# Performance work log

Hardware: AMD Instinct MI355X
Metric: run time of the kernel (lower is better)

The kernel has to match this reference:

```python
import jax, jax.numpy as jnp
import numpy as np

N = 10000        # nodes
E = 160000       # edges (avg degree 16)
WIDTH = 32       # node hidden width
KER_W = 256      # kernel MLP hidden width
KER_IN = 6       # edge feature dim
DEPTH = 4        # message-passing iterations


def setup_inputs() -> dict:
    key = jax.random.key(0)
    ks = jax.random.split(key, 12)
    def w(k, shape, fan_in):
        return jax.random.normal(k, shape, jnp.float32) * (1.0 / np.sqrt(fan_in)).astype(np.float32)
    return {
        "x": jax.random.normal(ks[0], (N, 1), jnp.float32),
        "edge_index": jax.random.randint(ks[1], (2, E), 0, N),
        "edge_attr": jax.random.uniform(ks[2], (E, KER_IN), dtype=jnp.float32),
        # fc1: Linear(1, WIDTH)
        "fc1_w": w(ks[3], (1, WIDTH), 1), "fc1_b": jnp.zeros((WIDTH,), jnp.float32),
        # kernel DenseNet: KER_IN -> KER_W -> KER_W -> WIDTH^2 (ReLU between, none after last)
        "k1_w": w(ks[4], (KER_IN, KER_W), KER_IN), "k1_b": jnp.zeros((KER_W,), jnp.float32),
        "k2_w": w(ks[5], (KER_W, KER_W), KER_W), "k2_b": jnp.zeros((KER_W,), jnp.float32),
        "k3_w": w(ks[6], (KER_W, WIDTH * WIDTH), KER_W), "k3_b": jnp.zeros((WIDTH * WIDTH,), jnp.float32),
        # NNConv root weight + bias
        "root_w": w(ks[7], (WIDTH, WIDTH), WIDTH), "conv_b": jnp.zeros((WIDTH,), jnp.float32),
        # fc2: Linear(WIDTH, 1)
        "fc2_w": w(ks[8], (WIDTH, 1), WIDTH), "fc2_b": jnp.zeros((1,), jnp.float32),
    }


def reference(x, edge_index, edge_attr, fc1_w, fc1_b, k1_w, k1_b, k2_w, k2_b,
              k3_w, k3_b, root_w, conv_b, fc2_w, fc2_b):
    src, dst = edge_index[0], edge_index[1]  # messages flow src -> dst

    # Per-edge kernel weights (edge_attr is constant across depth -> compute once).
    h = jax.nn.relu(edge_attr @ k1_w + k1_b)
    h = jax.nn.relu(h @ k2_w + k2_b)
    W_e = (h @ k3_w + k3_b).reshape(E, WIDTH, WIDTH)  # [E, in, out]

    # Degree for scatter-mean (avoid div by zero).
    deg = jax.ops.segment_sum(jnp.ones((E,), jnp.float32), dst, num_segments=N)
    inv_deg = (1.0 / jnp.maximum(deg, 1.0))[:, None]

    h_node = x @ fc1_w + fc1_b  # [N, WIDTH]
    for _ in range(DEPTH):
        msg = jnp.einsum('ei,eio->eo', h_node[src], W_e)              # gather + per-edge GEMM
        agg = jax.ops.segment_sum(msg, dst, num_segments=N) * inv_deg  # scatter-mean
        h_node = jax.nn.relu(agg + h_node @ root_w + conv_b)
    return h_node @ fc2_w + fc2_b  # [N, 1]
```

## Files before the change

kernel.cpp:

```cpp
#include <hip/hip_runtime.h>
#include <hip/hip_fp16.h>

#define NNODE 10000
#define NEDGE 160000
#define W32 32
#define BSTR 40
#define PANEL_F16 10240
#define PANEL3_F16 5120
#define UB_TILES 20000
#define HB_STR 268
#define TB_STR 1036

typedef _Float16 f16;
typedef _Float16 f16x4 __attribute__((ext_vector_type(4)));
typedef _Float16 f16x8 __attribute__((ext_vector_type(8)));
typedef float f32x4 __attribute__((ext_vector_type(4)));

__device__ __forceinline__ void stage_panel(f16* lds, const f16* g, int w, int lane) {
    #pragma unroll
    for (int i = 0; i < 5; ++i) {
        int slot = w * 320 + i * 64 + lane;
        __builtin_amdgcn_global_load_lds(
            (const __attribute__((address_space(1))) unsigned int*)(g + (size_t)slot * 8),
            (__attribute__((address_space(3))) unsigned int*)(lds + (size_t)(w * 320 + i * 64) * 8),
            16, 0, 0);
    }
}

__device__ __forceinline__ void stage_panel10k(f16* lds, const f16* g, int w, int lane) {
    #pragma unroll
    for (int i = 0; i < 2; ++i) {
        int base = i * 256 + w * 64;
        __builtin_amdgcn_global_load_lds(
            (const __attribute__((address_space(1))) unsigned int*)(g + (size_t)(base + lane) * 8),
            (__attribute__((address_space(3))) unsigned int*)(lds + (size_t)base * 8),
            16, 0, 0);
    }
    if (w < 2) {
        int base = 512 + w * 64;
        __builtin_amdgcn_global_load_lds(
            (const __attribute__((address_space(1))) unsigned int*)(g + (size_t)(base + lane) * 8),
            (__attribute__((address_space(3))) unsigned int*)(lds + (size_t)base * 8),
            16, 0, 0);
    }
}

__global__ __launch_bounds__(256) void pack_k1(const float* __restrict__ k1w, f16* __restrict__ k1p) {
    int t = blockIdx.x * 256 + threadIdx.x;
    int j = t / BSTR, c = t % BSTR;
    k1p[t] = (c < 6) ? (f16)k1w[c * 256 + j] : (f16)0.f;
}
__global__ __launch_bounds__(256) void pack_k2(const float* __restrict__ k2w, f16* __restrict__ k2p) {
    int t = blockIdx.x * 256 + threadIdx.x;
    int kk = t / PANEL_F16, r = t % PANEL_F16;
    int j = r / BSTR, c = r % BSTR;
    k2p[t] = (c < 32) ? (f16)k2w[(size_t)(kk * 32 + c) * 256 + j] : (f16)0.f;
}
__global__ __launch_bounds__(256) void pack_k3(const float* __restrict__ k3w, f16* __restrict__ k3p) {
    int t = blockIdx.x * 256 + threadIdx.x;
    int p = t / PANEL3_F16, r = t % PANEL3_F16;
    int np = p >> 3, kk = p & 7;
    int j = r / BSTR, c = r % BSTR;
    k3p[t] = (c < 32) ? (f16)k3w[(size_t)(kk * 32 + c) * 1024 + np * 128 + j] : (f16)0.f;
}
__global__ __launch_bounds__(256) void pack_k3t(const float* __restrict__ k3w, f16* __restrict__ k3t) {
    int t = blockIdx.x * 256 + threadIdx.x;
    int q = t / BSTR, i = t % BSTR;
    int o = q >> 8, c = q & 255;
    k3t[t] = (i < 32) ? (f16)k3w[(size_t)c * 1024 + i * 32 + o] : (f16)0.f;
}

__global__ __launch_bounds__(256) void h2_kernel(
    const float* __restrict__ ea,
    const f16* __restrict__ k1p, const float* __restrict__ k1b,
    const f16* __restrict__ k2p, const float* __restrict__ k2b,
    f16* __restrict__ h2c, int e_start, const int* __restrict__ remap)
{
    __shared__ __align__(16) f16 bls[2][256 * BSTR];
    __shared__ __align__(16) f16 ea_s[64 * BSTR];
    __shared__ __align__(16) f16 hbuf[64 * HB_STR];

    const int t = threadIdx.x, w = t >> 6, lane = t & 63, quad = lane >> 4, l15 = lane & 15;
    const int el0 = blockIdx.x * 64;
    const int e0 = e_start + el0;

    stage_panel(bls[0], k1p, w, lane);
    for (int i = t; i < 64 * BSTR; i += 256) {
        int e = i / BSTR, c = i % BSTR;
        ea_s[i] = (f16)((c < 6) ? ea[(size_t)(e0 + e) * 6 + c] : 0.f);
    }
    __syncthreads();

    f16x8 a1 = *(const f16x8*)&ea_s[(w * 16 + l15) * BSTR + quad * 8];
    f32x4 acc[16];
    #pragma unroll
    for (int nt = 0; nt < 16; ++nt) { float b = k1b[nt * 16 + l15]; acc[nt] = (f32x4){b, b, b, b}; }
    stage_panel(bls[1], k2p, w, lane);
    #pragma unroll
    for (int nt = 0; nt < 16; ++nt) {
        f16x8 bf = *(const f16x8*)&bls[0][(nt * 16 + l15) * BSTR + quad * 8];
        acc[nt] = __builtin_amdgcn_mfma_f32_16x16x32_f16(a1, bf, acc[nt], 0, 0, 0);
    }
    #pragma unroll
    for (int nt = 0; nt < 16; ++nt)
        #pragma unroll
        for (int r = 0; r < 4; ++r)
            hbuf[(w * 16 + quad * 4 + r) * HB_STR + nt * 16 + l15] = (f16)fmaxf(acc[nt][r], 0.f);
    __syncthreads();

    f16x8 a2[8];
    #pragma unroll
    for (int kk = 0; kk < 8; ++kk)
        a2[kk] = *(const f16x8*)&hbuf[(w * 16 + l15) * HB_STR + kk * 32 + quad * 8];
    #pragma unroll
    for (int nt = 0; nt < 16; ++nt) { float b = k2b[nt * 16 + l15]; acc[nt] = (f32x4){b, b, b, b}; }
    for (int kk = 0; kk < 8; ++kk) {
        if (kk < 7)
            stage_panel(bls[kk & 1], k2p + (size_t)(kk + 1) * PANEL_F16, w, lane);
        const f16* B = bls[(kk + 1) & 1];
        #pragma unroll
        for (int nt = 0; nt < 16; ++nt) {
            f16x8 bf = *(const f16x8*)&B[(nt * 16 + l15) * BSTR + quad * 8];
            acc[nt] = __builtin_amdgcn_mfma_f32_16x16x32_f16(a2[kk], bf, acc[nt], 0, 0, 0);
        }
        __syncthreads();
    }
    #pragma unroll
    for (int nt = 0; nt < 16; ++nt)
        #pragma unroll
        for (int r = 0; r < 4; ++r)
            hbuf[(w * 16 + quad * 4 + r) * HB_STR + nt * 16 + l15] = (f16)fmaxf(acc[nt][r], 0.f);
    __syncthreads();
    {
        const int row = t >> 2, u = t & 3;
        const size_t orow = remap ? (size_t)remap[e0 + row] : (size_t)(el0 + row);
        f16* gdst = h2c + orow * 256;
        const f16* lsrc = &hbuf[row * HB_STR];
        #pragma unroll
        for (int j = 0; j < 8; ++j) {
            int p = u + 4 * j;
            *(f16x8*)(gdst + p * 8) = *(const f16x8*)(lsrc + p * 8);
        }
    }
}

__global__ __launch_bounds__(256) void hist_kernel(const int* __restrict__ ei, int* __restrict__ cnt) {
    int e = blockIdx.x * 256 + threadIdx.x;
    if (e < NEDGE) atomicAdd(&cnt[ei[e]], 1);
}
__global__ __launch_bounds__(256) void scan_kernel(
    const int* __restrict__ cnt, int* __restrict__ edgeStart,
    int* __restrict__ tileStartN, int* __restrict__ cursor)
{
    __shared__ int pE[256], pT[256];
    const int t = threadIdx.x;
    int se = 0, st = 0;
    for (int k = 0; k < 40; ++k) {
        int n = t * 40 + k;
        if (n < NNODE) { int c = cnt[n]; se += c; st += (c + 15) >> 4; }
    }
    pE[t] = se; pT[t] = st;
    __syncthreads();
    if (t == 0) {
        int aE = 0, aT = 0;
        for (int i = 0; i < 256; ++i) { int tE = pE[i], tT = pT[i]; pE[i] = aE; pT[i] = aT; aE += tE; aT += tT; }
        tileStartN[NNODE] = aT;
    }
    __syncthreads();
    int oE = pE[t], oT = pT[t];
    for (int k = 0; k < 40; ++k) {
        int n = t * 40 + k;
        if (n < NNODE) {
            edgeStart[n] = oE; cursor[n] = oE; tileStartN[n] = oT;
            int c = cnt[n]; oE += c; oT += (c + 15) >> 4;
        }
    }
}
__global__ __launch_bounds__(256) void scatter_kernel(
    const int* __restrict__ ei, int* __restrict__ cursor,
    int* __restrict__ dstS, int* __restrict__ sortpos)
{
    int e = blockIdx.x * 256 + threadIdx.x;
    if (e < NEDGE) {
        int s = ei[e];
        int p = atomicAdd(&cursor[s], 1);
        dstS[p] = ei[NEDGE + e];
        sortpos[e] = p;
    }
}
__global__ __launch_bounds__(256) void tiles_kernel(
    const int* __restrict__ cnt, const int* __restrict__ edgeStart, const int* __restrict__ tileStartN,
    int* __restrict__ tileNode, int* __restrict__ tileE0, int* __restrict__ tileCnt)
{
    int n = blockIdx.x * 256 + threadIdx.x;
    if (n < NNODE) {
        int d = cnt[n], t0 = tileStartN[n], e0 = edgeStart[n];
        for (int k = 0; k * 16 < d; ++k) {
            int rem = d - k * 16;
            tileNode[t0 + k] = n;
            tileE0[t0 + k] = e0 + k * 16;
            tileCnt[t0 + k] = rem < 16 ? rem : 16;
        }
    }
}

__global__ __launch_bounds__(256) void bb_kernel(
    const float* __restrict__ h, const float* __restrict__ k3b, float* __restrict__ Bb)
{
    int idx = blockIdx.x * 256 + threadIdx.x;
    int n = idx >> 5, o = idx & 31;
    float s = 0.f;
    #pragma unroll
    for (int i = 0; i < 32; ++i)
        s += h[n * 32 + i] * k3b[i * 32 + o];
    Bb[idx] = s;
}

__global__ __launch_bounds__(256) void tgen_kernel(
    const float* __restrict__ h, const f16* __restrict__ k3t, f16* __restrict__ Tt,
    int n0, int n1)
{
    __shared__ __align__(16) f16 tbuf[16 * TB_STR];

    const int t = threadIdx.x, w = t >> 6, lane = t & 63, quad = lane >> 4, l15 = lane & 15;
    const int nBase = n0 + blockIdx.x * 16;
    const int colBase = blockIdx.y * 1024;

    f16x8 a;
    #pragma unroll
    for (int i = 0; i < 8; ++i) a[i] = (f16)0.f;
    int node = nBase + l15;
    if (node < n1) {
        const float4* hp = (const float4*)(h + (size_t)node * 32) + quad * 2;
        float4 v0 = hp[0], v1 = hp[1];
        a[0] = (f16)v0.x; a[1] = (f16)v0.y; a[2] = (f16)v0.z; a[3] = (f16)v0.w;
        a[4] = (f16)v1.x; a[5] = (f16)v1.y; a[6] = (f16)v1.z; a[7] = (f16)v1.w;
    }
    f32x4 acc[16];
    #pragma unroll
    for (int nt = 0; nt < 16; ++nt) {
        f16x8 bf = *(const f16x8*)&k3t[(size_t)(colBase + w * 256 + nt * 16 + l15) * BSTR + quad * 8];
        acc[nt] = __builtin_amdgcn_mfma_f32_16x16x32_f16(a, bf, (f32x4){0.f, 0.f, 0.f, 0.f}, 0, 0, 0);
    }
    #pragma unroll
    for (int nt = 0; nt < 16; ++nt)
        #pragma unroll
        for (int r = 0; r < 4; ++r)
            tbuf[(quad * 4 + r) * TB_STR + w * 256 + nt * 16 + l15] = (f16)acc[nt][r];
    __syncthreads();
    {
        const int row = t >> 4, u = t & 15;
        const int nd = nBase + row;
        if (nd < n1) {
            f16* gdst = Tt + (size_t)(nd - n0) * 8192 + colBase;
            const f16* lsrc = &tbuf[row * TB_STR];
            #pragma unroll
            for (int j = 0; j < 8; ++j) {
                int p = u + 16 * j;
                *(f16x8*)(gdst + p * 8) = *(const f16x8*)(lsrc + p * 8);
            }
        }
    }
}

__global__ __launch_bounds__(256) void msgT_kernel(
    const f16* __restrict__ h2s, const f16* __restrict__ Tt, const float* __restrict__ Bb,
    const int* __restrict__ tileNode, const int* __restrict__ tileE0, const int* __restrict__ tileCnt,
    const int* __restrict__ tileStartN, const int* __restrict__ dstS, float* __restrict__ agg,
    int n0, int n1)
{
    const int t = threadIdx.x, w = t >> 6, lane = t & 63, quad = lane >> 4, l15 = lane & 15;
    const int t0 = tileStartN[n0], t1 = tileStartN[n1];
    for (int tile = t0 + blockIdx.x * 4 + w; tile < t1; tile += gridDim.x * 4) {
        int n = tileNode[tile];
        int e0 = tileE0[tile], cnt = tileCnt[tile];
        const f16* Tn = Tt + (size_t)(n - n0) * 8192;
        f32x4 acc[2];
        #pragma unroll
        for (int nt = 0; nt < 2; ++nt) {
            float b = Bb[n * 32 + nt * 16 + l15];
            acc[nt] = (f32x4){b, b, b, b};
        }
        #pragma unroll
        for (int kk = 0; kk < 8; ++kk) {
            f16x8 a;
            #pragma unroll
            for (int i = 0; i < 8; ++i) a[i] = (f16)0.f;
            if (l15 < cnt)
                a = *(const f16x8*)&h2s[(size_t)(e0 + l15) * 256 + kk * 32 + quad * 8];
            #pragma unroll
            for (int nt = 0; nt < 2; ++nt) {
                f16x8 bf = *(const f16x8*)&Tn[(nt * 16 + l15) * 256 + kk * 32 + quad * 8];
                acc[nt] = __builtin_amdgcn_mfma_f32_16x16x32_f16(a, bf, acc[nt], 0, 0, 0);
            }
        }
        #pragma unroll
        for (int nt = 0; nt < 2; ++nt)
            #pragma unroll
            for (int r = 0; r < 4; ++r) {
                int er = quad * 4 + r;
                if (er < cnt)
                    atomicAdd(&agg[(size_t)dstS[e0 + er] * 32 + nt * 16 + l15], acc[nt][r]);
            }
    }
}

__global__ __launch_bounds__(256, 2) void msg_fused(
    const int* __restrict__ ei, const f16* __restrict__ h2c,
    const f16* __restrict__ k3p, const float* __restrict__ k3b,
    const float* __restrict__ h, float* __restrict__ agg, int e_start)
{
    __shared__ __align__(16) f16 bls[2][PANEL3_F16];
    __shared__ __align__(16) f16 h_s[256 * 36];
    __shared__ int dst_s[256];

    const int t = threadIdx.x, w = t >> 6, lane = t & 63, quad = lane >> 4, l15 = lane & 15;
    const int el0 = blockIdx.x * 256;
    const int e0 = e_start + el0;

    dst_s[t] = ei[NEDGE + e0 + t];
    {
        int srcn = ei[e0 + t];
        const float4* hr = (const float4*)(h + (size_t)srcn * 32);
        f16* dp = &h_s[t * 36];
        #pragma unroll
        for (int qq = 0; qq < 8; ++qq) {
            float4 v = hr[qq];
            dp[qq * 4 + 0] = (f16)v.x; dp[qq * 4 + 1] = (f16)v.y;
            dp[qq * 4 + 2] = (f16)v.z; dp[qq * 4 + 3] = (f16)v.w;
        }
    }
    stage_panel10k(bls[0], k3p, w, lane);

    float msg[4][4][2];
    #pragma unroll
    for (int m = 0; m < 4; ++m)
        #pragma unroll
        for (int r = 0; r < 4; ++r) { msg[m][r][0] = 0.f; msg[m][r][1] = 0.f; }

    f32x4 acc[4][8];
    __syncthreads();

    for (int it = 0; it < 64; ++it) {
        const int np = it >> 3, kk = it & 7;
        if (it) __syncthreads();
        if (it < 63) stage_panel10k(bls[(it + 1) & 1], k3p + (size_t)(it + 1) * PANEL3_F16, w, lane);

        f16x8 a[4];
        #pragma unroll
        for (int m = 0; m < 4; ++m)
            a[m] = *(const f16x8*)(h2c + (size_t)(el0 + w * 64 + m * 16 + l15) * 256 + kk * 32 + quad * 8);

        if (kk == 0) {
            #pragma unroll
            for (int nt = 0; nt < 8; ++nt) {
                float b = k3b[np * 128 + nt * 16 + l15];
                #pragma unroll
                for (int m = 0; m < 4; ++m) acc[m][nt] = (f32x4){b, b, b, b};
            }
        }
        const f16* B = bls[it & 1];
        #pragma unroll
        for (int nt = 0; nt < 8; ++nt) {
            f16x8 bf = *(const f16x8*)&B[(nt * 16 + l15) * BSTR + quad * 8];
            #pragma unroll
            for (int m = 0; m < 4; ++m)
                acc[m][nt] = __builtin_amdgcn_mfma_f32_16x16x32_f16(a[m], bf, acc[m][nt], 0, 0, 0);
        }
        if (kk == 7) {
            #pragma unroll
            for (int m = 0; m < 4; ++m)
                #pragma unroll
                for (int r = 0; r < 4; ++r) {
                    int row = w * 64 + m * 16 + quad * 4 + r;
                    f16x4 h4 = *(const f16x4*)&h_s[row * 36 + np * 4];
                    #pragma unroll
                    for (int nt = 0; nt < 8; ++nt)
                        msg[m][r][nt & 1] += (float)h4[nt >> 1] * acc[m][nt][r];
                }
        }
    }
    #pragma unroll
    for (int m = 0; m < 4; ++m)
        #pragma unroll
        for (int r = 0; r < 4; ++r) {
            int d = dst_s[w * 64 + m * 16 + quad * 4 + r];
            atomicAdd(&agg[d * W32 + l15],      msg[m][r][0]);
            atomicAdd(&agg[d * W32 + 16 + l15], msg[m][r][1]);
        }
}

__global__ __launch_bounds__(256) void h0_kernel(
    const float* __restrict__ x, const float* __restrict__ fc1w,
    const float* __restrict__ fc1b, float* __restrict__ h)
{
    int idx = blockIdx.x * 256 + threadIdx.x;
    int n = idx >> 5, j = idx & 31;
    h[idx] = x[n] * fc1w[j] + fc1b[j];
}

__global__ __launch_bounds__(256) void deg_kernel(
    const int* __restrict__ ei, float* __restrict__ deg)
{
    int e = blockIdx.x * 256 + threadIdx.x;
    if (e < NEDGE) atomicAdd(&deg[ei[NEDGE + e]], 1.f);
}

__global__ __launch_bounds__(256) void update_kernel(
    const float* __restrict__ h_old, float* __restrict__ h_new,
    float* __restrict__ agg, const float* __restrict__ deg,
    const float* __restrict__ rootw, const float* __restrict__ convb)
{
    __shared__ float rw[W32][W32 + 1];
    const int t = threadIdx.x;
    for (int q = t; q < W32 * W32; q += 256)
        rw[q >> 5][q & 31] = rootw[q];
    __syncthreads();
    const int nl = t >> 5, j = t & 31;
    const int n = blockIdx.x * 8 + nl;
    float hv = h_old[n * W32 + j];
    float acc = convb[j];
    #pragma unroll
    for (int k = 0; k < W32; ++k)
        acc += __shfl(hv, k, 32) * rw[k][j];
    float inv = 1.f / fmaxf(deg[n], 1.f);
    int idx = n * W32 + j;
    float a = agg[idx];
    agg[idx] = 0.f;
    h_new[idx] = fmaxf(a * inv + acc, 0.f);
}

__global__ __launch_bounds__(256) void out_kernel(
    const float* __restrict__ h, const float* __restrict__ fc2w,
    const float* __restrict__ fc2b, float* __restrict__ out)
{
    int n = blockIdx.x * 256 + threadIdx.x;
    if (n < NNODE) {
        float a = fc2b[0];
        #pragma unroll
        for (int j = 0; j < W32; ++j)
            a += h[n * W32 + j] * fc2w[j];
        out[n] = a;
    }
}

static inline size_t pad256(size_t x) { return (x + 255) & ~(size_t)255; }

extern "C" void kernel_launch(void* const* d_in, const int* in_sizes, int n_in,
                              void* d_out, int out_size, void* d_ws, size_t ws_size,
                              hipStream_t stream) {
    const float* x    = (const float*)d_in[0];
    const int*   ei   = (const int*)  d_in[1];
    const float* ea   = (const float*)d_in[2];
    const float* fc1w = (const float*)d_in[3];
    const float* fc1b = (const float*)d_in[4];
    const float* k1w  = (const float*)d_in[5];
    const float* k1b  = (const float*)d_in[6];
    const float* k2w  = (const float*)d_in[7];
    const float* k2b  = (const float*)d_in[8];
    const float* k3w  = (const float*)d_in[9];
    const float* k3b  = (const float*)d_in[10];
    const float* rootw= (const float*)d_in[11];
    const float* convb= (const float*)d_in[12];
    const float* fc2w = (const float*)d_in[13];
    const float* fc2b = (const float*)d_in[14];
    float* out = (float*)d_out;

    const size_t hbytes = (size_t)NNODE * W32 * 4;
    char* ws = (char*)d_ws;
    size_t off = 0;
    float* hA  = (float*)(ws + off); off += hbytes;
    float* hB  = (float*)(ws + off); off += hbytes;
    float* agg = (float*)(ws + off); off += hbytes;
    float* deg = (float*)(ws + off); off += 40960;
    f16*  k1p  = (f16*)(ws + off);   off += 20480;
    f16*  k2p  = (f16*)(ws + off);   off += 163840;
    f16*  k3p  = (f16*)(ws + off);   off += 655360;
    const size_t fixed = off;

    size_t toff = fixed;
    f16*  k3t      = (f16*)(ws + toff);  toff += pad256(8192 * BSTR * 2);
    int*  dstS     = (int*)(ws + toff);  toff += pad256((size_t)NEDGE * 4);
    int*  sortpos  = (int*)(ws + toff);  toff += pad256((size_t)NEDGE * 4);
    int*  cnt      = (int*)(ws + toff);  toff += pad256((size_t)NNODE * 4);
    int*  edgeStart= (int*)(ws + toff);  toff += pad256((size_t)NNODE * 4);
    int*  tileStartN=(int*)(ws + toff);  toff += pad256((size_t)(NNODE + 1) * 4);
    int*  cursor   = (int*)(ws + toff);  toff += pad256((size_t)NNODE * 4);
    int*  tileNode = (int*)(ws + toff);  toff += pad256((size_t)UB_TILES * 4);
    int*  tileE0   = (int*)(ws + toff);  toff += pad256((size_t)UB_TILES * 4);
    int*  tileCnt  = (int*)(ws + toff);  toff += pad256((size_t)UB_TILES * 4);
    float* Bb      = (float*)(ws + toff); toff += pad256((size_t)NNODE * 32 * 4);
    f16*  h2s      = (f16*)(ws + toff);  toff += pad256((size_t)NEDGE * 256 * 2);
    f16*  Tt       = (f16*)(ws + toff);

    int nc = 0, CS = 0;
    {
        const int cands[4] = {1, 2, 4, 8};
        for (int ci = 0; ci < 4; ++ci) {
            int c = cands[ci];
            int cs = ((NNODE + c - 1) / c + 15) & ~15;
            size_t tb = (size_t)cs * 8192 * 2;
            if (ws_size >= toff + tb) { nc = c; CS = cs; break; }
        }
    }

    hipMemsetAsync(deg, 0, (size_t)NNODE * 4, stream);
    hipMemsetAsync(agg, 0, (size_t)NNODE * W32 * 4, stream);

    pack_k1<<<40, 256, 0, stream>>>(k1w, k1p);
    pack_k2<<<320, 256, 0, stream>>>(k2w, k2p);

    h0_kernel<<<NNODE * W32 / 256, 256, 0, stream>>>(x, fc1w, fc1b, hA);
    deg_kernel<<<(NEDGE + 255) / 256, 256, 0, stream>>>(ei, deg);

    float* hcur = hA; float* hnext = hB;

    if (nc) {
        pack_k3t<<<1280, 256, 0, stream>>>(k3w, k3t);
        hipMemsetAsync(cnt, 0, (size_t)NNODE * 4, stream);
        hist_kernel<<<(NEDGE + 255) / 256, 256, 0, stream>>>(ei, cnt);
        scan_kernel<<<1, 256, 0, stream>>>(cnt, edgeStart, tileStartN, cursor);
        scatter_kernel<<<(NEDGE + 255) / 256, 256, 0, stream>>>(ei, cursor, dstS, sortpos);
        tiles_kernel<<<(NNODE + 255) / 256, 256, 0, stream>>>(cnt, edgeStart, tileStartN,
                                                              tileNode, tileE0, tileCnt);
        h2_kernel<<<NEDGE / 64, 256, 0, stream>>>(ea, k1p, k1b, k2p, k2b, h2s, 0, sortpos);

        for (int d = 0; d < 4; ++d) {
            bb_kernel<<<NNODE * 32 / 256, 256, 0, stream>>>(hcur, k3b, Bb);
            for (int ct = 0; ct < nc; ++ct) {
                int n0 = ct * CS;
                if (n0 >= NNODE) break;
                int n1 = n0 + CS; if (n1 > NNODE) n1 = NNODE;
                dim3 tg((n1 - n0 + 15) / 16, 8);
                tgen_kernel<<<tg, 256, 0, stream>>>(hcur, k3t, Tt, n0, n1);
                msgT_kernel<<<1280, 256, 0, stream>>>(h2s, Tt, Bb, tileNode, tileE0, tileCnt,
                                                      tileStartN, dstS, agg, n0, n1);
            }
            update_kernel<<<NNODE / 8, 256, 0, stream>>>(hcur, hnext, agg, deg, rootw, convb);
            float* tmp = hcur; hcur = hnext; hnext = tmp;
        }
    } else {
        f16* h2b = (f16*)(ws + fixed);
        pack_k3<<<1280, 256, 0, stream>>>(k3w, k3p);

        long long availC = 0;
        if (ws_size > fixed) availC = (long long)((ws_size - fixed) / 512);
        int C = (availC > NEDGE) ? NEDGE : (int)availC;
        C &= ~255;
        if (C < 256) return;

        const bool full = (C == NEDGE);
        if (full)
            h2_kernel<<<NEDGE / 64, 256, 0, stream>>>(ea, k1p, k1b, k2p, k2b, h2b, 0, nullptr);

        for (int d = 0; d < 4; ++d) {
            for (int es = 0; es < NEDGE; es += C) {
                int ce = (NEDGE - es < C) ? (NEDGE - es) : C;
                if (!full)
                    h2_kernel<<<ce / 64, 256, 0, stream>>>(ea, k1p, k1b, k2p, k2b, h2b, es, nullptr);
                msg_fused<<<ce / 256, 256, 0, stream>>>(ei, h2b, k3p, k3b, hcur, agg, es);
            }
            update_kernel<<<NNODE / 8, 256, 0, stream>>>(hcur, hnext, agg, deg, rootw, convb);
            float* tmp = hcur; hcur = hnext; hnext = tmp;
        }
    }
    out_kernel<<<(NNODE + 255) / 256, 256, 0, stream>>>(hcur, fc2w, fc2b, out);
}
```

Baseline: 627.2 us.

## Enlarge h2 blocks to 128 edges and reuse k3t fragments across node groups in tgen

h2_kernel now runs 512 threads over 128 edges per block, so each staged k1/k2 weight panel serves twice as many edges. Its output is written straight from registers to global memory, dropping the LDS round-trip and one barrier. tgen_kernel loads its k3t B fragments into registers once and loops over four 16-node groups per block, cutting repeated weight loads and the number of blocks. The risks are more register pressure and scattered 2-byte global stores in h2, and extra barriers inside the tgen loop.

```diff
diff --git a/kernel.cpp b/kernel.cpp
--- a/kernel.cpp
+++ b/kernel.cpp
@@ -26,6 +26,23 @@
             16, 0, 0);
     }
 }
+__device__ __forceinline__ void stage_panel512(f16* lds, const f16* g, int w, int lane) {
+    #pragma unroll
+    for (int i = 0; i < 2; ++i) {
+        int base = i * 512 + w * 64;
+        __builtin_amdgcn_global_load_lds(
+            (const __attribute__((address_space(1))) unsigned int*)(g + (size_t)(base + lane) * 8),
+            (__attribute__((address_space(3))) unsigned int*)(lds + (size_t)base * 8),
+            16, 0, 0);
+    }
+    if (w < 4) {
+        int base = 1024 + w * 64;
+        __builtin_amdgcn_global_load_lds(
+            (const __attribute__((address_space(1))) unsigned int*)(g + (size_t)(base + lane) * 8),
+            (__attribute__((address_space(3))) unsigned int*)(lds + (size_t)base * 8),
+            16, 0, 0);
+    }
+}
 
 __device__ __forceinline__ void stage_panel10k(f16* lds, const f16* g, int w, int lane) {
     #pragma unroll
@@ -70,22 +87,22 @@
     k3t[t] = (i < 32) ? (f16)k3w[(size_t)c * 1024 + i * 32 + o] : (f16)0.f;
 }
 
-__global__ __launch_bounds__(256) void h2_kernel(
+__global__ __launch_bounds__(512) void h2_kernel(
     const float* __restrict__ ea,
     const f16* __restrict__ k1p, const float* __restrict__ k1b,
     const f16* __restrict__ k2p, const float* __restrict__ k2b,
     f16* __restrict__ h2c, int e_start, const int* __restrict__ remap)
 {
     __shared__ __align__(16) f16 bls[2][256 * BSTR];
-    __shared__ __align__(16) f16 ea_s[64 * BSTR];
-    __shared__ __align__(16) f16 hbuf[64 * HB_STR];
+    __shared__ __align__(16) f16 ea_s[128 * BSTR];
+    __shared__ __align__(16) f16 hbuf[128 * HB_STR];
 
     const int t = threadIdx.x, w = t >> 6, lane = t & 63, quad = lane >> 4, l15 = lane & 15;
-    const int el0 = blockIdx.x * 64;
+    const int el0 = blockIdx.x * 128;
     const int e0 = e_start + el0;
 
-    stage_panel(bls[0], k1p, w, lane);
-    for (int i = t; i < 64 * BSTR; i += 256) {
+    stage_panel512(bls[0], k1p, w, lane);
+    for (int i = t; i < 128 * BSTR; i += 512) {
         int e = i / BSTR, c = i % BSTR;
         ea_s[i] = (f16)((c < 6) ? ea[(size_t)(e0 + e) * 6 + c] : 0.f);
     }
@@ -95,7 +112,7 @@
     f32x4 acc[16];
     #pragma unroll
     for (int nt = 0; nt < 16; ++nt) { float b = k1b[nt * 16 + l15]; acc[nt] = (f32x4){b, b, b, b}; }
-    stage_panel(bls[1], k2p, w, lane);
+    stage_panel512(bls[1], k2p, w, lane);
     #pragma unroll
     for (int nt = 0; nt < 16; ++nt) {
         f16x8 bf = *(const f16x8*)&bls[0][(nt * 16 + l15) * BSTR + quad * 8];
@@ -106,7 +123,6 @@
         #pragma unroll
         for (int r = 0; r < 4; ++r)
             hbuf[(w * 16 + quad * 4 + r) * HB_STR + nt * 16 + l15] = (f16)fmaxf(acc[nt][r], 0.f);
-    __syncthreads();
 
     f16x8 a2[8];
     #pragma unroll
@@ -114,9 +130,10 @@
         a2[kk] = *(const f16x8*)&hbuf[(w * 16 + l15) * HB_STR + kk * 32 + quad * 8];
     #pragma unroll
     for (int nt = 0; nt < 16; ++nt) { float b = k2b[nt * 16 + l15]; acc[nt] = (f32x4){b, b, b, b}; }
+    __syncthreads();
     for (int kk = 0; kk < 8; ++kk) {
         if (kk < 7)
-            stage_panel(bls[kk & 1], k2p + (size_t)(kk + 1) * PANEL_F16, w, lane);
+            stage_panel512(bls[kk & 1], k2p + (size_t)(kk + 1) * PANEL_F16, w, lane);
         const f16* B = bls[(kk + 1) & 1];
         #pragma unroll
         for (int nt = 0; nt < 16; ++nt) {
@@ -125,23 +142,17 @@
         }
         __syncthreads();
     }
+    size_t orow[4];
+    #pragma unroll
+    for (int r = 0; r < 4; ++r) {
+        int eoff = w * 16 + quad * 4 + r;
+        orow[r] = remap ? (size_t)remap[e0 + eoff] : (size_t)(el0 + eoff);
+    }
     #pragma unroll
     for (int nt = 0; nt < 16; ++nt)
         #pragma unroll
         for (int r = 0; r < 4; ++r)
-            hbuf[(w * 16 + quad * 4 + r) * HB_STR + nt * 16 + l15] = (f16)fmaxf(acc[nt][r], 0.f);
-    __syncthreads();
-    {
-        const int row = t >> 2, u = t & 3;
-        const size_t orow = remap ? (size_t)remap[e0 + row] : (size_t)(el0 + row);
-        f16* gdst = h2c + orow * 256;
-        const f16* lsrc = &hbuf[row * HB_STR];
-        #pragma unroll
-        for (int j = 0; j < 8; ++j) {
-            int p = u + 4 * j;
-            *(f16x8*)(gdst + p * 8) = *(const f16x8*)(lsrc + p * 8);
-        }
-    }
+            h2c[orow[r] * 256 + nt * 16 + l15] = (f16)fmaxf(acc[nt][r], 0.f);
 }
 
 __global__ __launch_bounds__(256) void hist_kernel(const int* __restrict__ ei, int* __restrict__ cnt) {
@@ -223,43 +234,51 @@
     __shared__ __align__(16) f16 tbuf[16 * TB_STR];
 
     const int t = threadIdx.x, w = t >> 6, lane = t & 63, quad = lane >> 4, l15 = lane & 15;
-    const int nBase = n0 + blockIdx.x * 16;
+    const int gBase = n0 + blockIdx.x * 64;
     const int colBase = blockIdx.y * 1024;
 
-    f16x8 a;
-    #pragma unroll
-    for (int i = 0; i < 8; ++i) a[i] = (f16)0.f;
-    int node = nBase + l15;
-    if (node < n1) {
-        const float4* hp = (const float4*)(h + (size_t)node * 32) + quad * 2;
-        float4 v0 = hp[0], v1 = hp[1];
-        a[0] = (f16)v0.x; a[1] = (f16)v0.y; a[2] = (f16)v0.z; a[3] = (f16)v0.w;
-        a[4] = (f16)v1.x; a[5] = (f16)v1.y; a[6] = (f16)v1.z; a[7] = (f16)v1.w;
-    }
-    f32x4 acc[16];
-    #pragma unroll
-    for (int nt = 0; nt < 16; ++nt) {
-        f16x8 bf = *(const f16x8*)&k3t[(size_t)(colBase + w * 256 + nt * 16 + l15) * BSTR + quad * 8];
-        acc[nt] = __builtin_amdgcn_mfma_f32_16x16x32_f16(a, bf, (f32x4){0.f, 0.f, 0.f, 0.f}, 0, 0, 0);
-    }
+    f16x8 bf[16];
     #pragma unroll
     for (int nt = 0; nt < 16; ++nt)
-        #pragma unroll
-        for (int r = 0; r < 4; ++r)
-            tbuf[(quad * 4 + r) * TB_STR + w * 256 + nt * 16 + l15] = (f16)acc[nt][r];
-    __syncthreads();
-    {
-        const int row = t >> 4, u = t & 15;
-        const int nd = nBase + row;
-        if (nd < n1) {
-            f16* gdst = Tt + (size_t)(nd - n0) * 8192 + colBase;
-            const f16* lsrc = &tbuf[row * TB_STR];
-            #pragma unroll
-            for (int j = 0; j < 8; ++j) {
-                int p = u + 16 * j;
-                *(f16x8*)(gdst + p * 8) = *(const f16x8*)(lsrc + p * 8);
+        bf[nt] = *(const f16x8*)&k3t[(size_t)(colBase + w * 256 + nt * 16 + l15) * BSTR + quad * 8];
+
+    for (int mg = 0; mg < 4; ++mg) {
+        const int nBase = gBase + mg * 16;
+        if (nBase >= n1) break;
+        f16x8 a;
+        #pragma unroll
+        for (int i = 0; i < 8; ++i) a[i] = (f16)0.f;
+        int node = nBase + l15;
+        if (node < n1) {
+            const float4* hp = (const float4*)(h + (size_t)node * 32) + quad * 2;
+            float4 v0 = hp[0], v1 = hp[1];
+            a[0] = (f16)v0.x; a[1] = (f16)v0.y; a[2] = (f16)v0.z; a[3] = (f16)v0.w;
+            a[4] = (f16)v1.x; a[5] = (f16)v1.y; a[6] = (f16)v1.z; a[7] = (f16)v1.w;
+        }
+        f32x4 acc[16];
+        #pragma unroll
+        for (int nt = 0; nt < 16; ++nt)
+            acc[nt] = __builtin_amdgcn_mfma_f32_16x16x32_f16(a, bf[nt], (f32x4){0.f, 0.f, 0.f, 0.f}, 0, 0, 0);
+        #pragma unroll
+        for (int nt = 0; nt < 16; ++nt)
+            #pragma unroll
+            for (int r = 0; r < 4; ++r)
+                tbuf[(quad * 4 + r) * TB_STR + w * 256 + nt * 16 + l15] = (f16)acc[nt][r];
+        __syncthreads();
+        {
+            const int row = t >> 4, u = t & 15;
+            const int nd = nBase + row;
+            if (nd < n1) {
+                f16* gdst = Tt + (size_t)(nd - n0) * 8192 + colBase;
+                const f16* lsrc = &tbuf[row * TB_STR];
+                #pragma unroll
+                for (int j = 0; j < 8; ++j) {
+                    int p = u + 16 * j;
+                    *(f16x8*)(gdst + p * 8) = *(const f16x8*)(lsrc + p * 8);
+                }
             }
         }
+        __syncthreads();
     }
 }
 
@@ -523,7 +542,7 @@
         scatter_kernel<<<(NEDGE + 255) / 256, 256, 0, stream>>>(ei, cursor, dstS, sortpos);
         tiles_kernel<<<(NNODE + 255) / 256, 256, 0, stream>>>(cnt, edgeStart, tileStartN,
                                                               tileNode, tileE0, tileCnt);
-        h2_kernel<<<NEDGE / 64, 256, 0, stream>>>(ea, k1p, k1b, k2p, k2b, h2s, 0, sortpos);
+        h2_kernel<<<NEDGE / 128, 512, 0, stream>>>(ea, k1p, k1b, k2p, k2b, h2s, 0, sortpos);
 
         for (int d = 0; d < 4; ++d) {
             bb_kernel<<<NNODE * 32 / 256, 256, 0, stream>>>(hcur, k3b, Bb);
@@ -531,7 +550,7 @@
                 int n0 = ct * CS;
                 if (n0 >= NNODE) break;
                 int n1 = n0 + CS; if (n1 > NNODE) n1 = NNODE;
-                dim3 tg((n1 - n0 + 15) / 16, 8);
+                dim3 tg((n1 - n0 + 63) / 64, 8);
                 tgen_kernel<<<tg, 256, 0, stream>>>(hcur, k3t, Tt, n0, n1);
                 msgT_kernel<<<1280, 256, 0, stream>>>(h2s, Tt, Bb, tileNode, tileE0, tileCnt,
                                                       tileStartN, dstS, agg, n0, n1);
@@ -551,13 +570,13 @@
 
         const bool full = (C == NEDGE);
         if (full)
-            h2_kernel<<<NEDGE / 64, 256, 0, stream>>>(ea, k1p, k1b, k2p, k2b, h2b, 0, nullptr);
+            h2_kernel<<<NEDGE / 128, 512, 0, stream>>>(ea, k1p, k1b, k2p, k2b, h2b, 0, nullptr);
 
         for (int d = 0; d < 4; ++d) {
             for (int es = 0; es < NEDGE; es += C) {
                 int ce = (NEDGE - es < C) ? (NEDGE - es) : C;
                 if (!full)
-                    h2_kernel<<<ce / 64, 256, 0, stream>>>(ea, k1p, k1b, k2p, k2b, h2b, es, nullptr);
+                    h2_kernel<<<ce / 128, 512, 0, stream>>>(ea, k1p, k1b, k2p, k2b, h2b, es, nullptr);
                 msg_fused<<<ce / 256, 256, 0, stream>>>(ei, h2b, k3p, k3b, hcur, agg, es);
             }
             update_kernel<<<NNODE / 8, 256, 0, stream>>>(hcur, hnext, agg, deg, rootw, convb);
```

Result: slower. 640.1 us (+2.1%).

## Retile second MLP layer as 2x2 warp grid and store results directly

Applied to the files above, without the earlier changes.

The second kernel-MLP GEMM is retiled so each warp computes a 32-row by 128-column block instead of 16 rows by 256 columns, which halves LDS B-fragment reads per MFMA because each B fragment now feeds two A rows. The final ReLU output is written straight from registers to global memory, dropping the LDS staging pass and its barrier. The direct stores are 2-byte scattered writes rather than 16-byte vectorized ones, which may hurt store coalescing. The hbuf stride also changes from 268 to 264.

```diff
diff --git a/kernel.cpp b/kernel.cpp
--- a/kernel.cpp
+++ b/kernel.cpp
@@ -8,7 +8,7 @@
 #define PANEL_F16 10240
 #define PANEL3_F16 5120
 #define UB_TILES 20000
-#define HB_STR 268
+#define HB_STR 264
 #define TB_STR 1036
 
 typedef _Float16 f16;
@@ -92,56 +92,65 @@
     __syncthreads();
 
     f16x8 a1 = *(const f16x8*)&ea_s[(w * 16 + l15) * BSTR + quad * 8];
-    f32x4 acc[16];
-    #pragma unroll
-    for (int nt = 0; nt < 16; ++nt) { float b = k1b[nt * 16 + l15]; acc[nt] = (f32x4){b, b, b, b}; }
-    stage_panel(bls[1], k2p, w, lane);
-    #pragma unroll
-    for (int nt = 0; nt < 16; ++nt) {
-        f16x8 bf = *(const f16x8*)&bls[0][(nt * 16 + l15) * BSTR + quad * 8];
-        acc[nt] = __builtin_amdgcn_mfma_f32_16x16x32_f16(a1, bf, acc[nt], 0, 0, 0);
-    }
-    #pragma unroll
-    for (int nt = 0; nt < 16; ++nt)
-        #pragma unroll
-        for (int r = 0; r < 4; ++r)
-            hbuf[(w * 16 + quad * 4 + r) * HB_STR + nt * 16 + l15] = (f16)fmaxf(acc[nt][r], 0.f);
-    __syncthreads();
-
-    f16x8 a2[8];
-    #pragma unroll
-    for (int kk = 0; kk < 8; ++kk)
-        a2[kk] = *(const f16x8*)&hbuf[(w * 16 + l15) * HB_STR + kk * 32 + quad * 8];
-    #pragma unroll
-    for (int nt = 0; nt < 16; ++nt) { float b = k2b[nt * 16 + l15]; acc[nt] = (f32x4){b, b, b, b}; }
+    {
+        f32x4 acc1[16];
+        #pragma unroll
+        for (int nt = 0; nt < 16; ++nt) { float b = k1b[nt * 16 + l15]; acc1[nt] = (f32x4){b, b, b, b}; }
+        stage_panel(bls[1], k2p, w, lane);
+        #pragma unroll
+        for (int nt = 0; nt < 16; ++nt) {
+            f16x8 bf = *(const f16x8*)&bls[0][(nt * 16 + l15) * BSTR + quad * 8];
+            acc1[nt] = __builtin_amdgcn_mfma_f32_16x16x32_f16(a1, bf, acc1[nt], 0, 0, 0);
+        }
+        #pragma unroll
+        for (int nt = 0; nt < 16; ++nt)
+            #pragma unroll
+            for (int r = 0; r < 4; ++r)
+                hbuf[(w * 16 + quad * 4 + r) * HB_STR + nt * 16 + l15] = (f16)fmaxf(acc1[nt][r], 0.f);
+    }
+    __syncthreads();
+
+    const int mh = w & 1, nh = w >> 1;
+    f16x8 a2[2][8];
+    #pragma unroll
+    for (int m = 0; m < 2; ++m)
+        #pragma unroll
+        for (int kk = 0; kk < 8; ++kk)
+            a2[m][kk] = *(const f16x8*)&hbuf[(mh * 32 + m * 16 + l15) * HB_STR + kk * 32 + quad * 8];
+    f32x4 acc[2][8];
+    #pragma unroll
+    for (int nt = 0; nt < 8; ++nt) {
+        float b = k2b[nh * 128 + nt * 16 + l15];
+        acc[0][nt] = (f32x4){b, b, b, b};
+        acc[1][nt] = (f32x4){b, b, b, b};
+    }
     for (int kk = 0; kk < 8; ++kk) {
         if (kk < 7)
             stage_panel(bls[kk & 1], k2p + (size_t)(kk + 1) * PANEL_F16, w, lane);
         const f16* B = bls[(kk + 1) & 1];
         #pragma unroll
-        for (int nt = 0; nt < 16; ++nt) {
-            f16x8 bf = *(const f16x8*)&B[(nt * 16 + l15) * BSTR + quad * 8];
-            acc[nt] = __builtin_amdgcn_mfma_f32_16x16x32_f16(a2[kk], bf, acc[nt], 0, 0, 0);
+        for (int nt = 0; nt < 8; ++nt) {
+            f16x8 bf = *(const f16x8*)&B[(nh * 128 + nt * 16 + l15) * BSTR + quad * 8];
+            acc[0][nt] = __builtin_amdgcn_mfma_f32_16x16x32_f16(a2[0][kk], bf, acc[0][nt], 0, 0, 0);
+            acc[1][nt] = __builtin_amdgcn_mfma_f32_16x16x32_f16(a2[1][kk], bf, acc[1][nt], 0, 0, 0);
         }
         __syncthreads();
     }
-    #pragma unroll
-    for (int nt = 0; nt < 16; ++nt)
-        #pragma unroll
-        for (int r = 0; r < 4; ++r)
-            hbuf[(w * 16 + quad * 4 + r) * HB_STR + nt * 16 + l15] = (f16)fmaxf(acc[nt][r], 0.f);
-    __syncthreads();
-    {
-        const int row = t >> 2, u = t & 3;
-        const size_t orow = remap ? (size_t)remap[e0 + row] : (size_t)(el0 + row);
-        f16* gdst = h2c + orow * 256;
-        const f16* lsrc = &hbuf[row * HB_STR];
-        #pragma unroll
-        for (int j = 0; j < 8; ++j) {
-            int p = u + 4 * j;
-            *(f16x8*)(gdst + p * 8) = *(const f16x8*)(lsrc + p * 8);
-        }
-    }
+    size_t orow[2][4];
+    #pragma unroll
+    for (int m = 0; m < 2; ++m)
+        #pragma unroll
+        for (int r = 0; r < 4; ++r) {
+            int row = mh * 32 + m * 16 + quad * 4 + r;
+            orow[m][r] = remap ? (size_t)remap[e0 + row] : (size_t)(el0 + row);
+        }
+    #pragma unroll
+    for (int m = 0; m < 2; ++m)
+        #pragma unroll
+        for (int nt = 0; nt < 8; ++nt)
+            #pragma unroll
+            for (int r = 0; r < 4; ++r)
+                h2c[orow[m][r] * 256 + nh * 128 + nt * 16 + l15] = (f16)fmaxf(acc[m][nt][r], 0.f);
 }
 
 __global__ __launch_bounds__(256) void hist_kernel(const int* __restrict__ ei, int* __restrict__ cnt) {
```

New measurement: 616.3 us. No clear change (-1.7%).
